# Performance work log

Hardware: AMD Instinct MI355X
Metric: run time of the kernel (lower is better)

## Reference

```python
import jax, jax.numpy as jnp
import numpy as np

N_TABLES = 26
ROWS = 100001   # n + 1 per EmbeddingBag
D = 64          # m_spa
B = 8192
L = 4           # fixed pooling factor per bag


def setup_inputs() -> dict:
    key = jax.random.key(0)
    ks = jax.random.split(key, 16)
    inp = {}
    inp["dense_x"] = jax.random.normal(ks[0], (B, 13), dtype=jnp.float32)
    # offsets: bag k starts at k*L (fixed pooling factor), same for every table
    inp["lS_o"] = jnp.tile(jnp.arange(B, dtype=jnp.int64) * L, (N_TABLES, 1))
    inp["lS_i"] = jax.random.randint(ks[1], (N_TABLES, B * L), 0, 100000).astype(jnp.int64)
    # embedding tables, uniform(-r, r) with r = sqrt(2/(n+m))
    r = (2.0 / (100000 + D)) ** 0.5
    inp["emb_tables"] = jax.random.uniform(ks[2], (N_TABLES, ROWS, D), dtype=jnp.float32, minval=-r, maxval=r)
    def lin(k, n_in, n_out):
        k1, k2 = jax.random.split(k)
        w = jax.random.normal(k1, (n_out, n_in), dtype=jnp.float32) * (2.0 / n_in) ** 0.5
        b = jax.random.uniform(k2, (n_out,), dtype=jnp.float32, minval=-n_in**-0.5, maxval=n_in**-0.5)
        return w, b
    inp["bot_w0"], inp["bot_b0"] = lin(ks[3], 13, 512)
    inp["bot_w1"], inp["bot_b1"] = lin(ks[4], 512, 256)
    inp["bot_w2"], inp["bot_b2"] = lin(ks[5], 256, 64)
    inp["top_w0"], inp["top_b0"] = lin(ks[6], 415, 512)
    inp["top_w1"], inp["top_b1"] = lin(ks[7], 512, 256)
    inp["top_w2"], inp["top_b2"] = lin(ks[8], 256, 1)
    return inp


def _dlrm(dense_x, lS_o, lS_i, emb_tables,
          bot_w0, bot_b0, bot_w1, bot_b1, bot_w2, bot_b2,
          top_w0, top_b0, top_w1, top_b1, top_w2, top_b2):
    # bottom MLP: Linear+ReLU for every layer (sigmoid_bot=-1)
    x = jax.nn.relu(dense_x @ bot_w0.T + bot_b0)
    x = jax.nn.relu(x @ bot_w1.T + bot_b1)
    x = jax.nn.relu(x @ bot_w2.T + bot_b2)          # [B, D]
    # EmbeddingBag mean pooling per table (fixed bag length L encoded by lS_o)
    idx = lS_i.reshape(N_TABLES, B, L)
    gathered = jax.vmap(lambda tab, ix: tab[ix])(emb_tables, idx)  # [T, B, L, D]
    ly = gathered.mean(axis=2)                       # [T, B, D]
    # dot interaction: T_feat = cat([x]+ly) -> [B, 27, D]
    T_feat = jnp.concatenate([x[None], ly], axis=0).transpose(1, 0, 2)
    Z = jnp.einsum('bnd,bmd->bnm', T_feat, T_feat)   # [B, 27, 27]
    li, lj = np.tril_indices(N_TABLES + 1, -1)       # strict lower triangle (offset=0)
    Zflat = Z[:, li, lj]                             # [B, 351]
    R = jnp.concatenate([x, Zflat], axis=1)          # [B, 415]
    # top MLP: sigmoid_top=2 -> loop breaks before appending Sigmoid -> last layer linear
    z = jax.nn.relu(R @ top_w0.T + top_b0)
    z = jax.nn.relu(z @ top_w1.T + top_b1)
    z = z @ top_w2.T + top_b2                        # [B, 1]
    return z.reshape(-1)


def reference(dense_x, lS_o, lS_i, emb_tables,
              bot_w0, bot_b0, bot_w1, bot_b1, bot_w2, bot_b2,
              top_w0, top_b0, top_w1, top_b1, top_w2, top_b2):
    return _dlrm(dense_x, lS_o, lS_i, emb_tables,
                 bot_w0, bot_b0, bot_w1, bot_b1, bot_w2, bot_b2,
                 top_w0, top_b0, top_w1, top_b1, top_w2, top_b2)
```

## Files before the change

### kernel.cpp

```cpp
#include <hip/hip_runtime.h>
#include <hip/hip_bf16.h>

typedef short bf16x8 __attribute__((ext_vector_type(8)));
typedef float f32x4 __attribute__((ext_vector_type(4)));

#define B_SZ 8192

__device__ __forceinline__ float relu_f(float v){ return v > 0.f ? v : 0.f; }

__device__ __forceinline__ f32x4 mfma16(bf16x8 a, bf16x8 b, f32x4 c){
  return __builtin_amdgcn_mfma_f32_16x16x32_bf16(a, b, c, 0, 0, 0);
}

__global__ __launch_bounds__(256) void conv_f2b(const float* __restrict__ s,
                                                __hip_bfloat16* __restrict__ d, int n){
  int i = blockIdx.x * 256 + threadIdx.x;
  if (i < n) d[i] = __float2bfloat16(s[i]);
}

__global__ __launch_bounds__(256) void conv_pad_tw0(const float* __restrict__ s,
                                                    __hip_bfloat16* __restrict__ d){
  int i = blockIdx.x * 256 + threadIdx.x;
  if (i >= 512 * 416) return;
  int r = i / 416, k = i - r * 416;
  float v = (k < 415) ? s[r * 415 + k] : 0.f;
  d[i] = __float2bfloat16(v);
}

__global__ __launch_bounds__(256) void bot0(const float* __restrict__ X,
    const float* __restrict__ W, const float* __restrict__ Bv,
    __hip_bfloat16* __restrict__ H){
  int n = threadIdx.x;
  int m0 = blockIdx.x * 16;
  float w0[13], w1[13];
#pragma unroll
  for (int k = 0; k < 13; k++){ w0[k] = W[n*13 + k]; w1[k] = W[(n+256)*13 + k]; }
  float b0 = Bv[n], b1 = Bv[n + 256];
  for (int mi = 0; mi < 16; mi++){
    int m = m0 + mi;
    float a0 = b0, a1 = b1;
#pragma unroll
    for (int k = 0; k < 13; k++){
      float xv = X[m*13 + k];
      a0 += xv * w0[k]; a1 += xv * w1[k];
    }
    H[(size_t)m*512 + n]       = __float2bfloat16(relu_f(a0));
    H[(size_t)m*512 + n + 256] = __float2bfloat16(relu_f(a1));
  }
}

__global__ __launch_bounds__(256) void embed(const int* __restrict__ I,
    const float* __restrict__ T, __hip_bfloat16* __restrict__ LY){
  int wid  = blockIdx.x * 4 + (threadIdx.x >> 6);
  int lane = threadIdx.x & 63;
  int t = wid >> 13;
  int b = wid & 8191;
  const int4 ix = *(const int4*)(I + ((size_t)t << 15) + (b << 2));
  const float* tab = T + (size_t)t * (100001ull * 64ull);
  float s = tab[(size_t)ix.x*64 + lane] + tab[(size_t)ix.y*64 + lane]
          + tab[(size_t)ix.z*64 + lane] + tab[(size_t)ix.w*64 + lane];
  LY[((size_t)wid << 6) + lane] = __float2bfloat16(s * 0.25f);
}

template<int NT>
__global__ __launch_bounds__(256) void gemm_br(const __hip_bfloat16* __restrict__ A,
    const __hip_bfloat16* __restrict__ W, const float* __restrict__ Bv,
    __hip_bfloat16* __restrict__ C, int N, int K, int ldc){
  int lane = threadIdx.x & 63;
  int wave = blockIdx.x * 4 + (threadIdx.x >> 6);
  int ntiles = N / (16 * NT);
  int mi = wave / ntiles, ni = wave % ntiles;
  int row = lane & 15, quad = lane >> 4;
  const __hip_bfloat16* Ap = A + (size_t)(mi*16 + row) * K + quad*8;
  const __hip_bfloat16* Wp[NT];
  f32x4 acc[NT];
#pragma unroll
  for (int t = 0; t < NT; t++){
    Wp[t] = W + (size_t)(ni*16*NT + t*16 + row) * K + quad*8;
    acc[t] = (f32x4){0.f, 0.f, 0.f, 0.f};
  }
  for (int k = 0; k < K; k += 32){
    bf16x8 a = *(const bf16x8*)(Ap + k);
#pragma unroll
    for (int t = 0; t < NT; t++){
      bf16x8 b = *(const bf16x8*)(Wp[t] + k);
      acc[t] = mfma16(a, b, acc[t]);
    }
  }
#pragma unroll
  for (int t = 0; t < NT; t++){
    int n = ni*16*NT + t*16 + row;
    float bn = Bv[n];
#pragma unroll
    for (int r = 0; r < 4; r++){
      int m = mi*16 + quad*4 + r;
      C[(size_t)m*ldc + n] = __float2bfloat16(relu_f(acc[t][r] + bn));
    }
  }
}

__global__ __launch_bounds__(256) void interact(const __hip_bfloat16* __restrict__ LY,
    __hip_bfloat16* __restrict__ R){
  int b    = blockIdx.x * 4 + (threadIdx.x >> 6);
  int lane = threadIdx.x & 63;
  int row = lane & 15, quad = lane >> 4;
  __hip_bfloat16* Rb = R + (size_t)b * 416;
  f32x4 a00 = {0,0,0,0}, a10 = {0,0,0,0}, a11 = {0,0,0,0};
#pragma unroll
  for (int k = 0; k < 64; k += 32){
    int ko = k + quad*8;
    const __hip_bfloat16* p0 = (row == 0)
        ? (const __hip_bfloat16*)(Rb + ko)
        : (LY + ((((size_t)(row - 1) << 13) + b) << 6) + ko);
    bf16x8 f0 = *(const bf16x8*)p0;
    bf16x8 f1 = {0,0,0,0,0,0,0,0};
    if (row < 11)
      f1 = *(const bf16x8*)(LY + ((((size_t)(row + 15) << 13) + b) << 6) + ko);
    a00 = mfma16(f0, f0, a00);
    a10 = mfma16(f1, f0, a10);
    a11 = mfma16(f1, f1, a11);
  }
#pragma unroll
  for (int r = 0; r < 4; r++){
    { int i = quad*4 + r, j = row;
      if (i > j) Rb[64 + i*(i-1)/2 + j] = __float2bfloat16(a00[r]); }
    { int i = 16 + quad*4 + r, j = row;
      if (i < 27) Rb[64 + i*(i-1)/2 + j] = __float2bfloat16(a10[r]); }
    { int i = 16 + quad*4 + r, j = 16 + row;
      if (i < 27 && i > j) Rb[64 + i*(i-1)/2 + j] = __float2bfloat16(a11[r]); }
  }
  if (lane == 0) Rb[415] = __float2bfloat16(0.f);
}

__global__ __launch_bounds__(256) void topdot(const __hip_bfloat16* __restrict__ H,
    const float* __restrict__ W, const float* __restrict__ Bv, float* __restrict__ O){
  int b    = blockIdx.x * 4 + (threadIdx.x >> 6);
  int lane = threadIdx.x & 63;
  const __hip_bfloat16* h = H + ((size_t)b << 8) + lane*4;
  float4 wv = *(const float4*)(W + lane*4);
  float acc = __bfloat162float(h[0])*wv.x + __bfloat162float(h[1])*wv.y
            + __bfloat162float(h[2])*wv.z + __bfloat162float(h[3])*wv.w;
#pragma unroll
  for (int o = 32; o; o >>= 1) acc += __shfl_xor(acc, o, 64);
  if (lane == 0) O[b] = acc + Bv[0];
}

extern "C" void kernel_launch(void* const* d_in, const int* in_sizes, int n_in,
                              void* d_out, int out_size, void* d_ws, size_t ws_size,
                              hipStream_t stream) {
  const float* dense_x = (const float*)d_in[0];
  const int*   lS_i    = (const int*)d_in[2];
  const float* tables  = (const float*)d_in[3];
  const float* bw0 = (const float*)d_in[4];  const float* bb0 = (const float*)d_in[5];
  const float* bw1 = (const float*)d_in[6];  const float* bb1 = (const float*)d_in[7];
  const float* bw2 = (const float*)d_in[8];  const float* bb2 = (const float*)d_in[9];
  const float* tw0 = (const float*)d_in[10]; const float* tb0 = (const float*)d_in[11];
  const float* tw1 = (const float*)d_in[12]; const float* tb1 = (const float*)d_in[13];
  const float* tw2 = (const float*)d_in[14]; const float* tb2 = (const float*)d_in[15];
  float* out = (float*)d_out;
  char* ws = (char*)d_ws;

  __hip_bfloat16* w1b  = (__hip_bfloat16*)(ws + 0);
  __hip_bfloat16* w2b  = (__hip_bfloat16*)(ws + 262144);
  __hip_bfloat16* tw0b = (__hip_bfloat16*)(ws + 294912);
  __hip_bfloat16* tw1b = (__hip_bfloat16*)(ws + 720896);
  __hip_bfloat16* h0   = (__hip_bfloat16*)(ws + 983040);
  __hip_bfloat16* h1   = (__hip_bfloat16*)(ws + 9371648);
  __hip_bfloat16* R    = (__hip_bfloat16*)(ws + 13565952);
  __hip_bfloat16* ly   = (__hip_bfloat16*)(ws + 20381696);
  __hip_bfloat16* h3   = h0;
  __hip_bfloat16* h4   = h1;

  conv_f2b<<<512, 256, 0, stream>>>(bw1, w1b, 256*512);
  conv_f2b<<< 64, 256, 0, stream>>>(bw2, w2b, 64*256);
  conv_pad_tw0<<<832, 256, 0, stream>>>(tw0, tw0b);
  conv_f2b<<<512, 256, 0, stream>>>(tw1, tw1b, 256*512);

  bot0<<<512, 256, 0, stream>>>(dense_x, bw0, bb0, h0);

  embed<<<26*8192/4, 256, 0, stream>>>(lS_i, tables, ly);

  gemm_br<4><<<512, 256, 0, stream>>>(h0, w1b, bb1, h1, 256, 512, 256);
  gemm_br<1><<<512, 256, 0, stream>>>(h1, w2b, bb2, R, 64, 256, 416);

  interact<<<8192/4, 256, 0, stream>>>(ly, R);

  gemm_br<4><<<1024, 256, 0, stream>>>(R, tw0b, tb0, h3, 512, 416, 512);
  gemm_br<4><<<512, 256, 0, stream>>>(h3, tw1b, tb1, h4, 256, 512, 256);
  topdot<<<8192/4, 256, 0, stream>>>(h4, tw2, tb2, out);

  (void)in_sizes; (void)n_in; (void)out_size; (void)ws_size;
}
```

Measured before the change: 880.4 us.

## Fuse prep kernels, embedding+interaction, and top MLP tail; template K

```diff
diff --git a/kernel.cpp b/kernel.cpp
--- a/kernel.cpp
+++ b/kernel.cpp
@@ -4,86 +4,80 @@
 typedef short bf16x8 __attribute__((ext_vector_type(8)));
 typedef float f32x4 __attribute__((ext_vector_type(4)));
 
-#define B_SZ 8192
-
 __device__ __forceinline__ float relu_f(float v){ return v > 0.f ? v : 0.f; }
 
 __device__ __forceinline__ f32x4 mfma16(bf16x8 a, bf16x8 b, f32x4 c){
   return __builtin_amdgcn_mfma_f32_16x16x32_bf16(a, b, c, 0, 0, 0);
 }
 
-__global__ __launch_bounds__(256) void conv_f2b(const float* __restrict__ s,
-                                                __hip_bfloat16* __restrict__ d, int n){
-  int i = blockIdx.x * 256 + threadIdx.x;
-  if (i < n) d[i] = __float2bfloat16(s[i]);
-}
-
-__global__ __launch_bounds__(256) void conv_pad_tw0(const float* __restrict__ s,
-                                                    __hip_bfloat16* __restrict__ d){
-  int i = blockIdx.x * 256 + threadIdx.x;
-  if (i >= 512 * 416) return;
-  int r = i / 416, k = i - r * 416;
-  float v = (k < 415) ? s[r * 415 + k] : 0.f;
-  d[i] = __float2bfloat16(v);
-}
-
-__global__ __launch_bounds__(256) void bot0(const float* __restrict__ X,
-    const float* __restrict__ W, const float* __restrict__ Bv,
-    __hip_bfloat16* __restrict__ H){
-  int n = threadIdx.x;
-  int m0 = blockIdx.x * 16;
-  float w0[13], w1[13];
-#pragma unroll
-  for (int k = 0; k < 13; k++){ w0[k] = W[n*13 + k]; w1[k] = W[(n+256)*13 + k]; }
-  float b0 = Bv[n], b1 = Bv[n + 256];
-  for (int mi = 0; mi < 16; mi++){
-    int m = m0 + mi;
-    float a0 = b0, a1 = b1;
-#pragma unroll
-    for (int k = 0; k < 13; k++){
-      float xv = X[m*13 + k];
-      a0 += xv * w0[k]; a1 += xv * w1[k];
-    }
-    H[(size_t)m*512 + n]       = __float2bfloat16(relu_f(a0));
-    H[(size_t)m*512 + n + 256] = __float2bfloat16(relu_f(a1));
-  }
-}
-
-__global__ __launch_bounds__(256) void embed(const int* __restrict__ I,
-    const float* __restrict__ T, __hip_bfloat16* __restrict__ LY){
-  int wid  = blockIdx.x * 4 + (threadIdx.x >> 6);
-  int lane = threadIdx.x & 63;
-  int t = wid >> 13;
-  int b = wid & 8191;
-  const int4 ix = *(const int4*)(I + ((size_t)t << 15) + (b << 2));
-  const float* tab = T + (size_t)t * (100001ull * 64ull);
-  float s = tab[(size_t)ix.x*64 + lane] + tab[(size_t)ix.y*64 + lane]
-          + tab[(size_t)ix.z*64 + lane] + tab[(size_t)ix.w*64 + lane];
-  LY[((size_t)wid << 6) + lane] = __float2bfloat16(s * 0.25f);
-}
-
-template<int NT>
+__device__ __forceinline__ short bfbits(float v){
+  __hip_bfloat16 h = __float2bfloat16(v);
+  return *reinterpret_cast<short*>(&h);
+}
+
+__global__ __launch_bounds__(256) void prep(
+    const float* __restrict__ X,  const float* __restrict__ bw0,
+    const float* __restrict__ bb0, __hip_bfloat16* __restrict__ H,
+    const float* __restrict__ bw1, __hip_bfloat16* __restrict__ w1b,
+    const float* __restrict__ bw2, __hip_bfloat16* __restrict__ w2b,
+    const float* __restrict__ tw0, __hip_bfloat16* __restrict__ tw0b,
+    const float* __restrict__ tw1, __hip_bfloat16* __restrict__ tw1b){
+  int blk = blockIdx.x;
+  if (blk < 512){
+    int n = threadIdx.x;
+    int m0 = blk * 16;
+    float w0[13], w1[13];
+#pragma unroll
+    for (int k = 0; k < 13; k++){ w0[k] = bw0[n*13 + k]; w1[k] = bw0[(n+256)*13 + k]; }
+    float b0 = bb0[n], b1 = bb0[n + 256];
+    for (int mi = 0; mi < 16; mi++){
+      int m = m0 + mi;
+      float a0 = b0, a1 = b1;
+#pragma unroll
+      for (int k = 0; k < 13; k++){
+        float xv = X[m*13 + k];
+        a0 += xv * w0[k]; a1 += xv * w1[k];
+      }
+      H[(size_t)m*512 + n]       = __float2bfloat16(relu_f(a0));
+      H[(size_t)m*512 + n + 256] = __float2bfloat16(relu_f(a1));
+    }
+  } else if (blk < 1024){
+    int i = (blk - 512)*256 + threadIdx.x;
+    w1b[i] = __float2bfloat16(bw1[i]);
+  } else if (blk < 1088){
+    int i = (blk - 1024)*256 + threadIdx.x;
+    w2b[i] = __float2bfloat16(bw2[i]);
+  } else if (blk < 1920){
+    int i = (blk - 1088)*256 + threadIdx.x;
+    int r = i / 416, k = i - r*416;
+    float v = (k < 415) ? tw0[r*415 + k] : 0.f;
+    tw0b[i] = __float2bfloat16(v);
+  } else {
+    int i = (blk - 1920)*256 + threadIdx.x;
+    tw1b[i] = __float2bfloat16(tw1[i]);
+  }
+}
+
+template<int NT, int K>
 __global__ __launch_bounds__(256) void gemm_br(const __hip_bfloat16* __restrict__ A,
     const __hip_bfloat16* __restrict__ W, const float* __restrict__ Bv,
-    __hip_bfloat16* __restrict__ C, int N, int K, int ldc){
+    __hip_bfloat16* __restrict__ C, int N, int ldc){
   int lane = threadIdx.x & 63;
   int wave = blockIdx.x * 4 + (threadIdx.x >> 6);
   int ntiles = N / (16 * NT);
   int mi = wave / ntiles, ni = wave % ntiles;
   int row = lane & 15, quad = lane >> 4;
   const __hip_bfloat16* Ap = A + (size_t)(mi*16 + row) * K + quad*8;
-  const __hip_bfloat16* Wp[NT];
+  const __hip_bfloat16* Wp = W + (size_t)(ni*16*NT + row) * K + quad*8;
   f32x4 acc[NT];
 #pragma unroll
-  for (int t = 0; t < NT; t++){
-    Wp[t] = W + (size_t)(ni*16*NT + t*16 + row) * K + quad*8;
-    acc[t] = (f32x4){0.f, 0.f, 0.f, 0.f};
-  }
+  for (int t = 0; t < NT; t++) acc[t] = (f32x4){0.f, 0.f, 0.f, 0.f};
+#pragma unroll
   for (int k = 0; k < K; k += 32){
     bf16x8 a = *(const bf16x8*)(Ap + k);
 #pragma unroll
     for (int t = 0; t < NT; t++){
-      bf16x8 b = *(const bf16x8*)(Wp[t] + k);
+      bf16x8 b = *(const bf16x8*)(Wp + (size_t)t*16*K + k);
       acc[t] = mfma16(a, b, acc[t]);
     }
   }
@@ -99,23 +93,54 @@
   }
 }
 
-__global__ __launch_bounds__(256) void interact(const __hip_bfloat16* __restrict__ LY,
-    __hip_bfloat16* __restrict__ R){
+__global__ __launch_bounds__(256) void embint(const int* __restrict__ I,
+    const float* __restrict__ T, __hip_bfloat16* __restrict__ R){
   int b    = blockIdx.x * 4 + (threadIdx.x >> 6);
   int lane = threadIdx.x & 63;
   int row = lane & 15, quad = lane >> 4;
   __hip_bfloat16* Rb = R + (size_t)b * 416;
+
+  int4 ix0 = {0,0,0,0}, ix1 = {0,0,0,0};
+  if (row >= 1) ix0 = *(const int4*)(I + ((size_t)(row - 1) << 15) + (b << 2));
+  if (row < 11) ix1 = *(const int4*)(I + ((size_t)(row + 15) << 15) + (b << 2));
+
   f32x4 a00 = {0,0,0,0}, a10 = {0,0,0,0}, a11 = {0,0,0,0};
 #pragma unroll
   for (int k = 0; k < 64; k += 32){
     int ko = k + quad*8;
-    const __hip_bfloat16* p0 = (row == 0)
-        ? (const __hip_bfloat16*)(Rb + ko)
-        : (LY + ((((size_t)(row - 1) << 13) + b) << 6) + ko);
-    bf16x8 f0 = *(const bf16x8*)p0;
-    bf16x8 f1 = {0,0,0,0,0,0,0,0};
-    if (row < 11)
-      f1 = *(const bf16x8*)(LY + ((((size_t)(row + 15) << 13) + b) << 6) + ko);
+    bf16x8 f0, f1 = {0,0,0,0,0,0,0,0};
+    if (row == 0){
+      f0 = *(const bf16x8*)(Rb + ko);
+    } else {
+      const float* tb = T + (size_t)(row - 1) * 6400064ull + ko;
+      float s[8] = {0,0,0,0,0,0,0,0};
+      int idx[4] = {ix0.x, ix0.y, ix0.z, ix0.w};
+#pragma unroll
+      for (int l = 0; l < 4; l++){
+        const float* p = tb + (size_t)idx[l]*64;
+        float4 u = *(const float4*)p;
+        float4 v = *(const float4*)(p + 4);
+        s[0]+=u.x; s[1]+=u.y; s[2]+=u.z; s[3]+=u.w;
+        s[4]+=v.x; s[5]+=v.y; s[6]+=v.z; s[7]+=v.w;
+      }
+#pragma unroll
+      for (int j = 0; j < 8; j++) f0[j] = bfbits(s[j]*0.25f);
+    }
+    if (row < 11){
+      const float* tb = T + (size_t)(row + 15) * 6400064ull + ko;
+      float s[8] = {0,0,0,0,0,0,0,0};
+      int idx[4] = {ix1.x, ix1.y, ix1.z, ix1.w};
+#pragma unroll
+      for (int l = 0; l < 4; l++){
+        const float* p = tb + (size_t)idx[l]*64;
+        float4 u = *(const float4*)p;
+        float4 v = *(const float4*)(p + 4);
+        s[0]+=u.x; s[1]+=u.y; s[2]+=u.z; s[3]+=u.w;
+        s[4]+=v.x; s[5]+=v.y; s[6]+=v.z; s[7]+=v.w;
+      }
+#pragma unroll
+      for (int j = 0; j < 8; j++) f1[j] = bfbits(s[j]*0.25f);
+    }
     a00 = mfma16(f0, f0, a00);
     a10 = mfma16(f1, f0, a10);
     a11 = mfma16(f1, f1, a11);
@@ -132,17 +157,56 @@
   if (lane == 0) Rb[415] = __float2bfloat16(0.f);
 }
 
-__global__ __launch_bounds__(256) void topdot(const __hip_bfloat16* __restrict__ H,
-    const float* __restrict__ W, const float* __restrict__ Bv, float* __restrict__ O){
-  int b    = blockIdx.x * 4 + (threadIdx.x >> 6);
-  int lane = threadIdx.x & 63;
-  const __hip_bfloat16* h = H + ((size_t)b << 8) + lane*4;
-  float4 wv = *(const float4*)(W + lane*4);
-  float acc = __bfloat162float(h[0])*wv.x + __bfloat162float(h[1])*wv.y
-            + __bfloat162float(h[2])*wv.z + __bfloat162float(h[3])*wv.w;
-#pragma unroll
-  for (int o = 32; o; o >>= 1) acc += __shfl_xor(acc, o, 64);
-  if (lane == 0) O[b] = acc + Bv[0];
+template<int K>
+__global__ __launch_bounds__(256) void top12(const __hip_bfloat16* __restrict__ A,
+    const __hip_bfloat16* __restrict__ W, const float* __restrict__ Bv,
+    const float* __restrict__ W2, const float* __restrict__ b2,
+    float* __restrict__ O){
+  __shared__ float part[4][16];
+  int lane = threadIdx.x & 63, wv = threadIdx.x >> 6;
+  int mi = blockIdx.x;
+  int row = lane & 15, quad = lane >> 4;
+  const __hip_bfloat16* Ap = A + (size_t)(mi*16 + row) * K + quad*8;
+  int nb = wv * 64;
+  const __hip_bfloat16* Wp = W + (size_t)(nb + row) * K + quad*8;
+  f32x4 acc[4];
+#pragma unroll
+  for (int t = 0; t < 4; t++) acc[t] = (f32x4){0.f, 0.f, 0.f, 0.f};
+#pragma unroll
+  for (int k = 0; k < K; k += 32){
+    bf16x8 a = *(const bf16x8*)(Ap + k);
+#pragma unroll
+    for (int t = 0; t < 4; t++){
+      bf16x8 b = *(const bf16x8*)(Wp + (size_t)t*16*K + k);
+      acc[t] = mfma16(a, b, acc[t]);
+    }
+  }
+  float p[4];
+#pragma unroll
+  for (int r = 0; r < 4; r++){
+    float s = 0.f;
+#pragma unroll
+    for (int t = 0; t < 4; t++){
+      int n = nb + t*16 + row;
+      s += relu_f(acc[t][r] + Bv[n]) * W2[n];
+    }
+    p[r] = s;
+  }
+#pragma unroll
+  for (int r = 0; r < 4; r++){
+#pragma unroll
+    for (int o = 1; o < 16; o <<= 1) p[r] += __shfl_xor(p[r], o, 64);
+  }
+  if (row == 0){
+#pragma unroll
+    for (int r = 0; r < 4; r++) part[wv][quad*4 + r] = p[r];
+  }
+  __syncthreads();
+  if (threadIdx.x < 16){
+    float s = part[0][threadIdx.x] + part[1][threadIdx.x]
+            + part[2][threadIdx.x] + part[3][threadIdx.x] + b2[0];
+    O[mi*16 + threadIdx.x] = s;
+  }
 }
 
 extern "C" void kernel_launch(void* const* d_in, const int* in_sizes, int n_in,
@@ -167,27 +231,15 @@
   __hip_bfloat16* h0   = (__hip_bfloat16*)(ws + 983040);
   __hip_bfloat16* h1   = (__hip_bfloat16*)(ws + 9371648);
   __hip_bfloat16* R    = (__hip_bfloat16*)(ws + 13565952);
-  __hip_bfloat16* ly   = (__hip_bfloat16*)(ws + 20381696);
   __hip_bfloat16* h3   = h0;
-  __hip_bfloat16* h4   = h1;
-
-  conv_f2b<<<512, 256, 0, stream>>>(bw1, w1b, 256*512);
-  conv_f2b<<< 64, 256, 0, stream>>>(bw2, w2b, 64*256);
-  conv_pad_tw0<<<832, 256, 0, stream>>>(tw0, tw0b);
-  conv_f2b<<<512, 256, 0, stream>>>(tw1, tw1b, 256*512);
-
-  bot0<<<512, 256, 0, stream>>>(dense_x, bw0, bb0, h0);
-
-  embed<<<26*8192/4, 256, 0, stream>>>(lS_i, tables, ly);
-
-  gemm_br<4><<<512, 256, 0, stream>>>(h0, w1b, bb1, h1, 256, 512, 256);
-  gemm_br<1><<<512, 256, 0, stream>>>(h1, w2b, bb2, R, 64, 256, 416);
-
-  interact<<<8192/4, 256, 0, stream>>>(ly, R);
-
-  gemm_br<4><<<1024, 256, 0, stream>>>(R, tw0b, tb0, h3, 512, 416, 512);
-  gemm_br<4><<<512, 256, 0, stream>>>(h3, tw1b, tb1, h4, 256, 512, 256);
-  topdot<<<8192/4, 256, 0, stream>>>(h4, tw2, tb2, out);
+
+  prep<<<2432, 256, 0, stream>>>(dense_x, bw0, bb0, h0,
+                                 bw1, w1b, bw2, w2b, tw0, tw0b, tw1, tw1b);
+  gemm_br<4,512><<<512, 256, 0, stream>>>(h0, w1b, bb1, h1, 256, 256);
+  gemm_br<1,256><<<512, 256, 0, stream>>>(h1, w2b, bb2, R, 64, 416);
+  embint<<<8192/4, 256, 0, stream>>>(lS_i, tables, R);
+  gemm_br<4,416><<<1024, 256, 0, stream>>>(R, tw0b, tb0, h3, 512, 512);
+  top12<512><<<512, 256, 0, stream>>>(h3, tw1b, tb1, tw2, tb2, out);
 
   (void)in_sizes; (void)n_in; (void)out_size; (void)ws_size;
 }
```

Result: faster. 846.2 us (-3.9%).
